# Performance work log

Hardware: AMD Instinct MI355X
Metric: run time of the kernel (lower is better)

## Reference

```python
import jax, jax.numpy as jnp
import numpy as np

N, V, T, C_IN, C_OUT, REL, H4, H5 = 256, 25, 128, 64, 64, 9, 18, 6


def setup_inputs() -> dict:
    key = jax.random.key(0)
    ks = jax.random.split(key, 12)

    def w(k, shape, fan_in):
        return (jax.random.normal(k, shape, jnp.float32) / np.sqrt(fan_in)).astype(jnp.float32)

    return {
        "x": jax.random.normal(ks[0], (N, V, T, C_IN), jnp.float32),
        "A": jax.random.uniform(ks[1], (V, V), dtype=jnp.float32),
        "W1": w(ks[2], (C_IN, REL), C_IN), "b1": jnp.zeros((REL,), jnp.float32),
        "W2": w(ks[3], (C_IN, REL), C_IN), "b2": jnp.zeros((REL,), jnp.float32),
        "W3": w(ks[4], (C_IN, REL), C_IN), "b3": jnp.zeros((REL,), jnp.float32),
        "W4a": w(ks[5], (REL, H4), REL), "b4a": jnp.zeros((H4,), jnp.float32),
        "W4b": w(ks[6], (H4, REL), H4), "b4b": jnp.zeros((REL,), jnp.float32),
        "W5a": w(ks[7], (REL, H5), REL), "b5a": jnp.zeros((H5,), jnp.float32),
        "W5b": w(ks[8], (H5, C_OUT), H5), "b5b": jnp.zeros((C_OUT,), jnp.float32),
    }


def reference(x, A, W1, b1, W2, b2, W3, b3, W4a, b4a, W4b, b4b, W5a, b5a, W5b, b5b):
    silu = jax.nn.silu
    alpha = 1.0
    # x: (N, V, T, C) channels-last; Linear projections to rel channels
    x1 = x @ W1 + b1                       # (N, V, T, R)
    x2 = x @ W2 + b2                       # (N, V, T, R)
    x3 = x @ W3 + b3                       # (N, V, T, R)
    # temporal mean (original: transpose(1,3).mean(-2))
    m1 = x1.mean(axis=2)                   # (N, V, R)
    m2 = x2.mean(axis=2)                   # (N, V, R)
    # pairwise joint affinity via broadcast difference
    rel = m1[:, :, None, :] - m2[:, None, :, :]   # (N, V, V, R)
    # small MLP (Linear4) on channel dim
    h = silu(rel @ W4a + b4a)              # (N, V, V, 18)
    h = silu(h @ W4b + b4b)                # (N, V, V, R)
    # scale + static adjacency (broadcast over batch and channels)
    h = h * alpha + A[None, :, :, None]    # (N, V, V, R)
    # einsum 'ncuv,nctv->nctu' in channels-last form: aggregate over v
    agg = jnp.einsum('nuvc,nvtc->nutc', h, x3)    # (N, V, T, R)
    # output MLP (Linear5)
    y = silu(agg @ W5a + b5a)              # (N, V, T, 6)
    y = silu(y @ W5b + b5b)                # (N, V, T, C_out)
    return y
```

## Files before the change

### kernel.cpp

```cpp
#include <hip/hip_runtime.h>
#include <hip/hip_fp16.h>

#define NN 256
#define VV 25
#define TT 128
#define CIN 64
#define CO 64
#define RR 9
#define HH4 18
#define HH5 6
#define TQ 32
#define NT 4

typedef unsigned int uint;

__device__ __forceinline__ float silu_f(float v) {
  return __fdividef(v, 1.0f + __expf(-v));
}
__device__ __forceinline__ __half2 u2h(uint u) {
  union { uint x; __half2 h; } c; c.x = u; return c.h;
}
__device__ __forceinline__ uint h2u(__half2 h) {
  union { __half2 h; uint x; } c; c.h = h; return c.x;
}

__global__ __launch_bounds__(128, 2) void k1_proj(
    const float* __restrict__ x, const float* __restrict__ W3,
    const float* __restrict__ b3, uint* __restrict__ x3g,
    float* __restrict__ xm) {
  const int blk = blockIdx.x;
  const int n = blk / VV, v = blk - n * VV;
  const int tid = threadIdx.x;
  __shared__ __align__(16) float xt[TT * 68];
  __shared__ __align__(16) float xmp[2][64];

  const float4* src = (const float4*)(x + (size_t)blk * TT * CIN);
  float4 r[16];
  #pragma unroll
  for (int k = 0; k < 16; ++k) r[k] = src[k * 128 + tid];
  #pragma unroll
  for (int k = 0; k < 16; ++k) {
    const int idx = k * 128 + tid;
    const int t = idx >> 4, c = (idx & 15) * 4;
    *(float4*)(xt + t * 68 + c) = r[k];
  }
  float4 cs = r[0];
  #pragma unroll
  for (int k = 1; k < 16; ++k) {
    cs.x += r[k].x; cs.y += r[k].y; cs.z += r[k].z; cs.w += r[k].w;
  }
  #pragma unroll
  for (int m = 16; m < 64; m <<= 1) {
    cs.x += __shfl_xor(cs.x, m); cs.y += __shfl_xor(cs.y, m);
    cs.z += __shfl_xor(cs.z, m); cs.w += __shfl_xor(cs.w, m);
  }
  if ((tid & 63) < 16) *(float4*)(&xmp[tid >> 6][(tid & 15) * 4]) = cs;
  __syncthreads();
  if (tid < 64) xm[(size_t)blk * 64 + tid] = xmp[0][tid] + xmp[1][tid];

  float acc[RR];
  #pragma unroll
  for (int j = 0; j < RR; ++j) acc[j] = b3[j];
  const float* xrow = xt + tid * 68;
  #pragma unroll
  for (int c4 = 0; c4 < 16; ++c4) {
    const float4 xv = *(const float4*)(xrow + c4 * 4);
    #pragma unroll
    for (int j = 0; j < RR; ++j) {
      acc[j] = fmaf(xv.x, W3[(c4 * 4 + 0) * RR + j], acc[j]);
      acc[j] = fmaf(xv.y, W3[(c4 * 4 + 1) * RR + j], acc[j]);
      acc[j] = fmaf(xv.z, W3[(c4 * 4 + 2) * RR + j], acc[j]);
      acc[j] = fmaf(xv.w, W3[(c4 * 4 + 3) * RR + j], acc[j]);
    }
  }
  uint w[5];
  w[0] = h2u(__floats2half2_rn(acc[0], acc[1]));
  w[1] = h2u(__floats2half2_rn(acc[2], acc[3]));
  w[2] = h2u(__floats2half2_rn(acc[4], acc[5]));
  w[3] = h2u(__floats2half2_rn(acc[6], acc[7]));
  w[4] = h2u(__floats2half2_rn(acc[8], 0.f));
  const int tq = tid >> 5, t = tid & 31;
  uint* dst = x3g + (size_t)(n * NT + tq) * (5 * VV * TQ) + v * TQ + t;
  #pragma unroll
  for (int c = 0; c < 5; ++c) dst[c * (VV * TQ)] = w[c];
}

__global__ __launch_bounds__(256, 4) void k3_out(
    const uint* __restrict__ x3g, const float* __restrict__ xm,
    const float* __restrict__ A,
    const float* __restrict__ W1, const float* __restrict__ b1,
    const float* __restrict__ W2, const float* __restrict__ b2,
    const float* __restrict__ W4a, const float* __restrict__ b4a,
    const float* __restrict__ W4b, const float* __restrict__ b4b,
    const float* __restrict__ W5a, const float* __restrict__ b5a,
    const float* __restrict__ W5b, const float* __restrict__ b5b,
    float* __restrict__ out) {
  const int bid = blockIdx.x;
  const int n = bid >> 2, tq = bid & 3;
  const int tid = threadIdx.x;
  __shared__ __align__(16) uint pool[9525];
  uint* x3s = pool;
  uint* a5s = pool + 4000;
  float* m12 = (float*)(pool + 4000);
  float* xmL = (float*)(pool + 4500);
  uint* h_lds = pool + 6400;

  {
    const uint4* xsrc = (const uint4*)(x3g + (size_t)bid * 4000);
    for (int i = tid; i < 1000; i += 256) ((uint4*)x3s)[i] = xsrc[i];
    const float4* msrc = (const float4*)(xm + (size_t)n * VV * CIN);
    for (int i = tid; i < 400; i += 256) ((float4*)xmL)[i] = msrc[i];
  }
  __syncthreads();

  for (int i = tid; i < 2 * VV * RR; i += 256) {
    const int which = (i >= VV * RR);
    const int idx = which ? i - VV * RR : i;
    const int v = idx / RR, c = idx - v * RR;
    const float* W = which ? W2 : W1;
    const float* b = which ? b2 : b1;
    const float* row = xmL + v * CIN;
    float s = 0.f;
    #pragma unroll
    for (int k = 0; k < CIN; ++k) s = fmaf(row[k], W[k * RR + c], s);
    m12[(which * VV + v) * 10 + c] = s * (1.0f / TT) + b[c];
  }
  __syncthreads();

  for (int p = tid; p < VV * VV; p += 256) {
    const int u = p / VV, v2 = p - u * VV;
    float rel[RR];
    #pragma unroll
    for (int j = 0; j < RR; ++j) rel[j] = m12[u * 10 + j] - m12[(VV + v2) * 10 + j];
    float t1[HH4];
    #pragma unroll
    for (int k = 0; k < HH4; ++k) {
      float s = b4a[k];
      #pragma unroll
      for (int j = 0; j < RR; ++j) s = fmaf(rel[j], W4a[j * HH4 + k], s);
      t1[k] = silu_f(s);
    }
    const float av = A[u * VV + v2];
    float hc[RR];
    #pragma unroll
    for (int j = 0; j < RR; ++j) {
      float s = b4b[j];
      #pragma unroll
      for (int k = 0; k < HH4; ++k) s = fmaf(t1[k], W4b[k * RR + j], s);
      hc[j] = silu_f(s) + av;
    }
    uint* hp = h_lds + p * 5;
    hp[0] = h2u(__floats2half2_rn(hc[0], hc[1]));
    hp[1] = h2u(__floats2half2_rn(hc[2], hc[3]));
    hp[2] = h2u(__floats2half2_rn(hc[4], hc[5]));
    hp[3] = h2u(__floats2half2_rn(hc[6], hc[7]));
    hp[4] = h2u(__floats2half2_rn(hc[8], 0.f));
  }
  __syncthreads();

  for (int p = tid; p < VV * TQ; p += 256) {
    const int u = p >> 5, t = p & 31;
    const uint* hr = h_lds + u * VV * 5;
    __half2 c0 = u2h(0u), c1 = c0, c2 = c0, c3 = c0, c4 = c0;
    #pragma unroll 5
    for (int v2 = 0; v2 < VV; ++v2) {
      const int xo = v2 * TQ + t;
      const uint x0 = x3s[xo];
      const uint x1 = x3s[xo + 800];
      const uint x2 = x3s[xo + 1600];
      const uint x3 = x3s[xo + 2400];
      const uint x4 = x3s[xo + 3200];
      const uint* hv = hr + v2 * 5;
      c0 = __hfma2(u2h(hv[0]), u2h(x0), c0);
      c1 = __hfma2(u2h(hv[1]), u2h(x1), c1);
      c2 = __hfma2(u2h(hv[2]), u2h(x2), c2);
      c3 = __hfma2(u2h(hv[3]), u2h(x3), c3);
      c4 = __hfma2(u2h(hv[4]), u2h(x4), c4);
    }
    float ag[RR];
    ag[0] = __low2float(c0); ag[1] = __high2float(c0);
    ag[2] = __low2float(c1); ag[3] = __high2float(c1);
    ag[4] = __low2float(c2); ag[5] = __high2float(c2);
    ag[6] = __low2float(c3); ag[7] = __high2float(c3);
    ag[8] = __low2float(c4);
    float a5v[HH5];
    #pragma unroll
    for (int k = 0; k < HH5; ++k) {
      float s = b5a[k];
      #pragma unroll
      for (int j = 0; j < RR; ++j) s = fmaf(ag[j], W5a[j * HH5 + k], s);
      a5v[k] = silu_f(s);
    }
    a5s[p * 3 + 0] = h2u(__floats2half2_rn(a5v[0], a5v[1]));
    a5s[p * 3 + 1] = h2u(__floats2half2_rn(a5v[2], a5v[3]));
    a5s[p * 3 + 2] = h2u(__floats2half2_rn(a5v[4], a5v[5]));
  }
  __syncthreads();

  const int cq = (tid & 15) * 4;
  float4 wb[HH5];
  #pragma unroll
  for (int k = 0; k < HH5; ++k) wb[k] = *(const float4*)(W5b + k * CO + cq);
  const float4 bb = *(const float4*)(b5b + cq);
  for (int it = 0; it < (VV * TQ) / 16; ++it) {
    const int q = it * 16 + (tid >> 4);
    const int u = q >> 5, t = q & 31;
    const __half2 p01 = u2h(a5s[q * 3 + 0]);
    const __half2 p23 = u2h(a5s[q * 3 + 1]);
    const __half2 p45 = u2h(a5s[q * 3 + 2]);
    const float a0 = __low2float(p01), a1 = __high2float(p01);
    const float a2 = __low2float(p23), a3 = __high2float(p23);
    const float a4 = __low2float(p45), a5 = __high2float(p45);
    float4 y;
    y.x = silu_f(bb.x + a0 * wb[0].x + a1 * wb[1].x + a2 * wb[2].x +
                 a3 * wb[3].x + a4 * wb[4].x + a5 * wb[5].x);
    y.y = silu_f(bb.y + a0 * wb[0].y + a1 * wb[1].y + a2 * wb[2].y +
                 a3 * wb[3].y + a4 * wb[4].y + a5 * wb[5].y);
    y.z = silu_f(bb.z + a0 * wb[0].z + a1 * wb[1].z + a2 * wb[2].z +
                 a3 * wb[3].z + a4 * wb[4].z + a5 * wb[5].z);
    y.w = silu_f(bb.w + a0 * wb[0].w + a1 * wb[1].w + a2 * wb[2].w +
                 a3 * wb[3].w + a4 * wb[4].w + a5 * wb[5].w);
    float* orow = out +
        ((size_t)(n * VV + u) * TT + tq * TQ + t) * CO + cq;
    *(float4*)orow = y;
  }
}

extern "C" void kernel_launch(void* const* d_in, const int* in_sizes, int n_in,
                              void* d_out, int out_size, void* d_ws, size_t ws_size,
                              hipStream_t stream) {
  const float* x   = (const float*)d_in[0];
  const float* A   = (const float*)d_in[1];
  const float* W1  = (const float*)d_in[2];
  const float* b1  = (const float*)d_in[3];
  const float* W2  = (const float*)d_in[4];
  const float* b2  = (const float*)d_in[5];
  const float* W3  = (const float*)d_in[6];
  const float* b3  = (const float*)d_in[7];
  const float* W4a = (const float*)d_in[8];
  const float* b4a = (const float*)d_in[9];
  const float* W4b = (const float*)d_in[10];
  const float* b4b = (const float*)d_in[11];
  const float* W5a = (const float*)d_in[12];
  const float* b5a = (const float*)d_in[13];
  const float* W5b = (const float*)d_in[14];
  const float* b5b = (const float*)d_in[15];
  float* out = (float*)d_out;

  char* ws = (char*)d_ws;
  uint*  x3g = (uint*)ws;
  float* xm  = (float*)(ws + 16384000);

  hipLaunchKernelGGL(k1_proj, dim3(NN * VV), dim3(128), 0, stream,
                     x, W3, b3, x3g, xm);
  hipLaunchKernelGGL(k3_out, dim3(NN * NT), dim3(256), 0, stream,
                     x3g, xm, A, W1, b1, W2, b2, W4a, b4a, W4b, b4b,
                     W5a, b5a, W5b, b5b, out);
}
```

Measured before the change: 174.4 us.

## Split fused output kernel into separate h, aggregation, and output-MLP kernels

The single k3_out kernel is split into three launches. k2_h computes the per-batch pairwise affinity h once per batch instead of once per time quarter and stores it to global memory. k3_agg does the aggregation and first output layer and writes a 6-wide intermediate to global memory. k4_out runs the final 6-to-64 layer with a higher occupancy bound. This removes the fourfold redundant h computation and lowers LDS pressure, at the cost of extra launches and an intermediate written to and read back from global memory.

```diff
diff --git a/kernel.cpp b/kernel.cpp
--- a/kernel.cpp
+++ b/kernel.cpp
@@ -85,53 +85,37 @@
   for (int c = 0; c < 5; ++c) dst[c * (VV * TQ)] = w[c];
 }
 
-__global__ __launch_bounds__(256, 4) void k3_out(
-    const uint* __restrict__ x3g, const float* __restrict__ xm,
-    const float* __restrict__ A,
+__global__ __launch_bounds__(128) void k2_h(
+    const float* __restrict__ xm, const float* __restrict__ A,
     const float* __restrict__ W1, const float* __restrict__ b1,
     const float* __restrict__ W2, const float* __restrict__ b2,
     const float* __restrict__ W4a, const float* __restrict__ b4a,
     const float* __restrict__ W4b, const float* __restrict__ b4b,
-    const float* __restrict__ W5a, const float* __restrict__ b5a,
-    const float* __restrict__ W5b, const float* __restrict__ b5b,
-    float* __restrict__ out) {
-  const int bid = blockIdx.x;
-  const int n = bid >> 2, tq = bid & 3;
-  const int tid = threadIdx.x;
-  __shared__ __align__(16) uint pool[9525];
-  uint* x3s = pool;
-  uint* a5s = pool + 4000;
-  float* m12 = (float*)(pool + 4000);
-  float* xmL = (float*)(pool + 4500);
-  uint* h_lds = pool + 6400;
-
-  {
-    const uint4* xsrc = (const uint4*)(x3g + (size_t)bid * 4000);
-    for (int i = tid; i < 1000; i += 256) ((uint4*)x3s)[i] = xsrc[i];
-    const float4* msrc = (const float4*)(xm + (size_t)n * VV * CIN);
-    for (int i = tid; i < 400; i += 256) ((float4*)xmL)[i] = msrc[i];
-  }
-  __syncthreads();
-
-  for (int i = tid; i < 2 * VV * RR; i += 256) {
+    uint* __restrict__ h2g) {
+  const int n = blockIdx.x;
+  const int tid = threadIdx.x;
+  __shared__ float m1[VV][RR + 1];
+  __shared__ float m2[VV][RR + 1];
+  const float* xmn = xm + (size_t)n * VV * CIN;
+  for (int i = tid; i < 2 * VV * RR; i += 128) {
     const int which = (i >= VV * RR);
     const int idx = which ? i - VV * RR : i;
     const int v = idx / RR, c = idx - v * RR;
     const float* W = which ? W2 : W1;
     const float* b = which ? b2 : b1;
-    const float* row = xmL + v * CIN;
+    const float* row = xmn + v * CIN;
     float s = 0.f;
     #pragma unroll
     for (int k = 0; k < CIN; ++k) s = fmaf(row[k], W[k * RR + c], s);
-    m12[(which * VV + v) * 10 + c] = s * (1.0f / TT) + b[c];
+    s = s * (1.0f / TT) + b[c];
+    if (which) m2[v][c] = s; else m1[v][c] = s;
   }
   __syncthreads();
-
-  for (int p = tid; p < VV * VV; p += 256) {
+  for (int p = tid; p < VV * VV; p += 128) {
     const int u = p / VV, v2 = p - u * VV;
     float rel[RR];
     #pragma unroll
-    for (int j = 0; j < RR; ++j) rel[j] = m12[u * 10 + j] - m12[(VV + v2) * 10 + j];
+    for (int j = 0; j < RR; ++j) rel[j] = m1[u][j] - m2[v2][j];
     float t1[HH4];
     #pragma unroll
     for (int k = 0; k < HH4; ++k) {
@@ -149,18 +133,36 @@
       for (int k = 0; k < HH4; ++k) s = fmaf(t1[k], W4b[k * RR + j], s);
       hc[j] = silu_f(s) + av;
     }
-    uint* hp = h_lds + p * 5;
+    uint* hp = h2g + (size_t)n * (VV * VV * 5) + (size_t)p * 5;
     hp[0] = h2u(__floats2half2_rn(hc[0], hc[1]));
     hp[1] = h2u(__floats2half2_rn(hc[2], hc[3]));
     hp[2] = h2u(__floats2half2_rn(hc[4], hc[5]));
     hp[3] = h2u(__floats2half2_rn(hc[6], hc[7]));
     hp[4] = h2u(__floats2half2_rn(hc[8], 0.f));
   }
+}
+
+__global__ __launch_bounds__(256, 4) void k3_agg(
+    const uint* __restrict__ x3g, const uint* __restrict__ h2g,
+    const float* __restrict__ W5a, const float* __restrict__ b5a,
+    float* __restrict__ a5g) {
+  const int bid = blockIdx.x;
+  const int n = bid >> 2, tq = bid & 3;
+  const int tid = threadIdx.x;
+  __shared__ __align__(16) uint x3s[5 * VV * TQ];
+  __shared__ __align__(16) uint h2s[VV * VV * 5];
+
+  {
+    const uint4* xsrc = (const uint4*)(x3g + (size_t)bid * 4000);
+    for (int i = tid; i < 1000; i += 256) ((uint4*)x3s)[i] = xsrc[i];
+    const uint* hsrc = h2g + (size_t)n * (VV * VV * 5);
+    for (int i = tid; i < VV * VV * 5; i += 256) h2s[i] = hsrc[i];
+  }
   __syncthreads();
 
   for (int p = tid; p < VV * TQ; p += 256) {
     const int u = p >> 5, t = p & 31;
-    const uint* hr = h_lds + u * VV * 5;
+    const uint* hr = h2s + u * (VV * 5);
     __half2 c0 = u2h(0u), c1 = c0, c2 = c0, c3 = c0, c4 = c0;
     #pragma unroll 5
     for (int v2 = 0; v2 < VV; ++v2) {
@@ -191,38 +193,39 @@
       for (int j = 0; j < RR; ++j) s = fmaf(ag[j], W5a[j * HH5 + k], s);
       a5v[k] = silu_f(s);
     }
-    a5s[p * 3 + 0] = h2u(__floats2half2_rn(a5v[0], a5v[1]));
-    a5s[p * 3 + 1] = h2u(__floats2half2_rn(a5v[2], a5v[3]));
-    a5s[p * 3 + 2] = h2u(__floats2half2_rn(a5v[4], a5v[5]));
-  }
-  __syncthreads();
-
+    const size_t row = ((size_t)(n * VV + u)) * TT + tq * TQ + t;
+    float* dst = a5g + row * 8;
+    *(float4*)dst = make_float4(a5v[0], a5v[1], a5v[2], a5v[3]);
+    *(float2*)(dst + 4) = make_float2(a5v[4], a5v[5]);
+  }
+}
+
+__global__ __launch_bounds__(256, 8) void k4_out(
+    const float* __restrict__ a5g,
+    const float* __restrict__ W5b, const float* __restrict__ b5b,
+    float* __restrict__ out) {
+  const int tid = threadIdx.x;
   const int cq = (tid & 15) * 4;
   float4 wb[HH5];
   #pragma unroll
   for (int k = 0; k < HH5; ++k) wb[k] = *(const float4*)(W5b + k * CO + cq);
   const float4 bb = *(const float4*)(b5b + cq);
-  for (int it = 0; it < (VV * TQ) / 16; ++it) {
-    const int q = it * 16 + (tid >> 4);
-    const int u = q >> 5, t = q & 31;
-    const __half2 p01 = u2h(a5s[q * 3 + 0]);
-    const __half2 p23 = u2h(a5s[q * 3 + 1]);
-    const __half2 p45 = u2h(a5s[q * 3 + 2]);
-    const float a0 = __low2float(p01), a1 = __high2float(p01);
-    const float a2 = __low2float(p23), a3 = __high2float(p23);
-    const float a4 = __low2float(p45), a5 = __high2float(p45);
+  const size_t row0 = (size_t)blockIdx.x * 400 + (tid >> 4);
+  #pragma unroll 2
+  for (int it = 0; it < 25; ++it) {
+    const size_t r = row0 + (size_t)it * 16;
+    const float4 aA = *(const float4*)(a5g + r * 8);
+    const float2 aB = *(const float2*)(a5g + r * 8 + 4);
     float4 y;
-    y.x = silu_f(bb.x + a0 * wb[0].x + a1 * wb[1].x + a2 * wb[2].x +
-                 a3 * wb[3].x + a4 * wb[4].x + a5 * wb[5].x);
-    y.y = silu_f(bb.y + a0 * wb[0].y + a1 * wb[1].y + a2 * wb[2].y +
-                 a3 * wb[3].y + a4 * wb[4].y + a5 * wb[5].y);
-    y.z = silu_f(bb.z + a0 * wb[0].z + a1 * wb[1].z + a2 * wb[2].z +
-                 a3 * wb[3].z + a4 * wb[4].z + a5 * wb[5].z);
-    y.w = silu_f(bb.w + a0 * wb[0].w + a1 * wb[1].w + a2 * wb[2].w +
-                 a3 * wb[3].w + a4 * wb[4].w + a5 * wb[5].w);
-    float* orow = out +
-        ((size_t)(n * VV + u) * TT + tq * TQ + t) * CO + cq;
-    *(float4*)orow = y;
+    y.x = silu_f(bb.x + aA.x * wb[0].x + aA.y * wb[1].x + aA.z * wb[2].x +
+                 aA.w * wb[3].x + aB.x * wb[4].x + aB.y * wb[5].x);
+    y.y = silu_f(bb.y + aA.x * wb[0].y + aA.y * wb[1].y + aA.z * wb[2].y +
+                 aA.w * wb[3].y + aB.x * wb[4].y + aB.y * wb[5].y);
+    y.z = silu_f(bb.z + aA.x * wb[0].z + aA.y * wb[1].z + aA.z * wb[2].z +
+                 aA.w * wb[3].z + aB.x * wb[4].z + aB.y * wb[5].z);
+    y.w = silu_f(bb.w + aA.x * wb[0].w + aA.y * wb[1].w + aA.z * wb[2].w +
+                 aA.w * wb[3].w + aB.x * wb[4].w + aB.y * wb[5].w);
+    *(float4*)(out + r * CO + cq) = y;
   }
 }
 
@@ -250,10 +253,15 @@
   char* ws = (char*)d_ws;
   uint*  x3g = (uint*)ws;
   float* xm  = (float*)(ws + 16384000);
+  uint*  h2g = (uint*)(ws + 16384000 + 1638400);
+  float* a5g = (float*)(ws + 16384000 + 1638400 + 3200000);
 
   hipLaunchKernelGGL(k1_proj, dim3(NN * VV), dim3(128), 0, stream,
                      x, W3, b3, x3g, xm);
-  hipLaunchKernelGGL(k3_out, dim3(NN * NT), dim3(256), 0, stream,
-                     x3g, xm, A, W1, b1, W2, b2, W4a, b4a, W4b, b4b,
-                     W5a, b5a, W5b, b5b, out);
-}
+  hipLaunchKernelGGL(k2_h, dim3(NN), dim3(128), 0, stream,
+                     xm, A, W1, b1, W2, b2, W4a, b4a, W4b, b4b, h2g);
+  hipLaunchKernelGGL(k3_agg, dim3(NN * NT), dim3(256), 0, stream,
+                     x3g, h2g, W5a, b5a, a5g);
+  hipLaunchKernelGGL(k4_out, dim3(2048), dim3(256), 0, stream,
+                     a5g, W5b, b5b, out);
+}
```

Result: no change. 174.1 us (-0.2%).

## Split pairwise affinity MLP into its own kernel and halve output time tiles

Applied to the files above, without the earlier changes.

Moves the per-batch m1/m2 projection and pairwise MLP out of the output kernel into a new per-batch kernel that writes the half-precision affinity matrix to workspace. Before, every time-quarter block recomputed it redundantly. The output kernel now uses 16-step time tiles over 8 blocks per batch, reading the affinity directly from global memory, which gives more, lighter blocks. The projection kernel stages x in LDS as half precision to shrink shared memory, at some accuracy cost. The change also adds an extra kernel launch and a global round trip for the affinity data.

```diff
diff --git a/kernel.cpp b/kernel.cpp
--- a/kernel.cpp
+++ b/kernel.cpp
@@ -9,8 +9,8 @@
 #define RR 9
 #define HH4 18
 #define HH5 6
-#define TQ 32
-#define NT 4
+#define TQ 16
+#define NT 8
 
 typedef unsigned int uint;
 
@@ -24,14 +24,14 @@
   union { __half2 h; uint x; } c; c.h = h; return c.x;
 }
 
-__global__ __launch_bounds__(128, 2) void k1_proj(
+__global__ __launch_bounds__(128) void k1_proj(
     const float* __restrict__ x, const float* __restrict__ W3,
     const float* __restrict__ b3, uint* __restrict__ x3g,
     float* __restrict__ xm) {
   const int blk = blockIdx.x;
   const int n = blk / VV, v = blk - n * VV;
   const int tid = threadIdx.x;
-  __shared__ __align__(16) float xt[TT * 68];
+  __shared__ __align__(16) __half xt[TT * 66];
   __shared__ __align__(16) float xmp[2][64];
 
   const float4* src = (const float4*)(x + (size_t)blk * TT * CIN);
@@ -42,7 +42,8 @@
   for (int k = 0; k < 16; ++k) {
     const int idx = k * 128 + tid;
     const int t = idx >> 4, c = (idx & 15) * 4;
-    *(float4*)(xt + t * 68 + c) = r[k];
+    *(__half2*)(&xt[t * 66 + c])     = __floats2half2_rn(r[k].x, r[k].y);
+    *(__half2*)(&xt[t * 66 + c + 2]) = __floats2half2_rn(r[k].z, r[k].w);
   }
   float4 cs = r[0];
   #pragma unroll
@@ -61,16 +62,15 @@
   float acc[RR];
   #pragma unroll
   for (int j = 0; j < RR; ++j) acc[j] = b3[j];
-  const float* xrow = xt + tid * 68;
-  #pragma unroll
-  for (int c4 = 0; c4 < 16; ++c4) {
-    const float4 xv = *(const float4*)(xrow + c4 * 4);
+  const __half* xrow = xt + tid * 66;
+  #pragma unroll 8
+  for (int c2 = 0; c2 < 32; ++c2) {
+    const __half2 hv = *(const __half2*)(&xrow[c2 * 2]);
+    const float x0 = __low2float(hv), x1 = __high2float(hv);
     #pragma unroll
     for (int j = 0; j < RR; ++j) {
-      acc[j] = fmaf(xv.x, W3[(c4 * 4 + 0) * RR + j], acc[j]);
-      acc[j] = fmaf(xv.y, W3[(c4 * 4 + 1) * RR + j], acc[j]);
-      acc[j] = fmaf(xv.z, W3[(c4 * 4 + 2) * RR + j], acc[j]);
-      acc[j] = fmaf(xv.w, W3[(c4 * 4 + 3) * RR + j], acc[j]);
+      acc[j] = fmaf(x0, W3[(c2 * 2 + 0) * RR + j], acc[j]);
+      acc[j] = fmaf(x1, W3[(c2 * 2 + 1) * RR + j], acc[j]);
     }
   }
   uint w[5];
@@ -79,59 +79,43 @@
   w[2] = h2u(__floats2half2_rn(acc[4], acc[5]));
   w[3] = h2u(__floats2half2_rn(acc[6], acc[7]));
   w[4] = h2u(__floats2half2_rn(acc[8], 0.f));
-  const int tq = tid >> 5, t = tid & 31;
+  const int tq = tid >> 4, t = tid & 15;
   uint* dst = x3g + (size_t)(n * NT + tq) * (5 * VV * TQ) + v * TQ + t;
   #pragma unroll
   for (int c = 0; c < 5; ++c) dst[c * (VV * TQ)] = w[c];
 }
 
-__global__ __launch_bounds__(256, 4) void k3_out(
-    const uint* __restrict__ x3g, const float* __restrict__ xm,
-    const float* __restrict__ A,
+__global__ __launch_bounds__(128) void k2_h(
+    const float* __restrict__ xm, const float* __restrict__ A,
     const float* __restrict__ W1, const float* __restrict__ b1,
     const float* __restrict__ W2, const float* __restrict__ b2,
     const float* __restrict__ W4a, const float* __restrict__ b4a,
     const float* __restrict__ W4b, const float* __restrict__ b4b,
-    const float* __restrict__ W5a, const float* __restrict__ b5a,
-    const float* __restrict__ W5b, const float* __restrict__ b5b,
-    float* __restrict__ out) {
-  const int bid = blockIdx.x;
-  const int n = bid >> 2, tq = bid & 3;
+    uint* __restrict__ h2g) {
+  const int n = blockIdx.x;
   const int tid = threadIdx.x;
-  __shared__ __align__(16) uint pool[9525];
-  uint* x3s = pool;
-  uint* a5s = pool + 4000;
-  float* m12 = (float*)(pool + 4000);
-  float* xmL = (float*)(pool + 4500);
-  uint* h_lds = pool + 6400;
-
-  {
-    const uint4* xsrc = (const uint4*)(x3g + (size_t)bid * 4000);
-    for (int i = tid; i < 1000; i += 256) ((uint4*)x3s)[i] = xsrc[i];
-    const float4* msrc = (const float4*)(xm + (size_t)n * VV * CIN);
-    for (int i = tid; i < 400; i += 256) ((float4*)xmL)[i] = msrc[i];
-  }
-  __syncthreads();
-
-  for (int i = tid; i < 2 * VV * RR; i += 256) {
+  __shared__ float m1[VV][RR + 1];
+  __shared__ float m2[VV][RR + 1];
+  const float* xmn = xm + (size_t)n * VV * CIN;
+  for (int i = tid; i < 2 * VV * RR; i += 128) {
     const int which = (i >= VV * RR);
     const int idx = which ? i - VV * RR : i;
     const int v = idx / RR, c = idx - v * RR;
     const float* W = which ? W2 : W1;
     const float* b = which ? b2 : b1;
-    const float* row = xmL + v * CIN;
+    const float* row = xmn + v * CIN;
     float s = 0.f;
     #pragma unroll
     for (int k = 0; k < CIN; ++k) s = fmaf(row[k], W[k * RR + c], s);
-    m12[(which * VV + v) * 10 + c] = s * (1.0f / TT) + b[c];
-  }
-  __syncthreads();
-
-  for (int p = tid; p < VV * VV; p += 256) {
+    s = s * (1.0f / TT) + b[c];
+    if (which) m2[v][c] = s; else m1[v][c] = s;
+  }
+  __syncthreads();
+  for (int p = tid; p < VV * VV; p += 128) {
     const int u = p / VV, v2 = p - u * VV;
     float rel[RR];
     #pragma unroll
-    for (int j = 0; j < RR; ++j) rel[j] = m12[u * 10 + j] - m12[(VV + v2) * 10 + j];
+    for (int j = 0; j < RR; ++j) rel[j] = m1[u][j] - m2[v2][j];
     float t1[HH4];
     #pragma unroll
     for (int k = 0; k < HH4; ++k) {
@@ -149,27 +133,46 @@
       for (int k = 0; k < HH4; ++k) s = fmaf(t1[k], W4b[k * RR + j], s);
       hc[j] = silu_f(s) + av;
     }
-    uint* hp = h_lds + p * 5;
+    uint* hp = h2g + (size_t)n * (VV * VV * 5) + (size_t)p * 5;
     hp[0] = h2u(__floats2half2_rn(hc[0], hc[1]));
     hp[1] = h2u(__floats2half2_rn(hc[2], hc[3]));
     hp[2] = h2u(__floats2half2_rn(hc[4], hc[5]));
     hp[3] = h2u(__floats2half2_rn(hc[6], hc[7]));
     hp[4] = h2u(__floats2half2_rn(hc[8], 0.f));
   }
+}
+
+__global__ __launch_bounds__(256) void k3_out(
+    const uint* __restrict__ x3g, const uint* __restrict__ h2g,
+    const float* __restrict__ W5a, const float* __restrict__ b5a,
+    const float* __restrict__ W5b, const float* __restrict__ b5b,
+    float* __restrict__ out) {
+  const int bid = blockIdx.x;
+  const int n = bid >> 3, tq = bid & 7;
+  const int tid = threadIdx.x;
+  __shared__ __align__(16) uint x3s[5 * VV * TQ];
+  __shared__ __align__(16) uint a5s[VV * TQ * 3];
+
+  {
+    const uint4* xsrc = (const uint4*)(x3g + (size_t)bid * (5 * VV * TQ));
+    for (int i = tid; i < (5 * VV * TQ) / 4; i += 256)
+      ((uint4*)x3s)[i] = xsrc[i];
+  }
   __syncthreads();
 
   for (int p = tid; p < VV * TQ; p += 256) {
-    const int u = p >> 5, t = p & 31;
-    const uint* hr = h_lds + u * VV * 5;
+    const int u = p >> 4, t = p & 15;
+    const uint* hr = h2g + (size_t)n * (VV * VV * 5) + u * (VV * 5);
+    const uint* xr = x3s + t;
     __half2 c0 = u2h(0u), c1 = c0, c2 = c0, c3 = c0, c4 = c0;
     #pragma unroll 5
     for (int v2 = 0; v2 < VV; ++v2) {
-      const int xo = v2 * TQ + t;
-      const uint x0 = x3s[xo];
-      const uint x1 = x3s[xo + 800];
-      const uint x2 = x3s[xo + 1600];
-      const uint x3 = x3s[xo + 2400];
-      const uint x4 = x3s[xo + 3200];
+      const int xo = v2 * TQ;
+      const uint x0 = xr[xo];
+      const uint x1 = xr[xo + 400];
+      const uint x2 = xr[xo + 800];
+      const uint x3 = xr[xo + 1200];
+      const uint x4 = xr[xo + 1600];
       const uint* hv = hr + v2 * 5;
       c0 = __hfma2(u2h(hv[0]), u2h(x0), c0);
       c1 = __hfma2(u2h(hv[1]), u2h(x1), c1);
@@ -204,7 +207,7 @@
   const float4 bb = *(const float4*)(b5b + cq);
   for (int it = 0; it < (VV * TQ) / 16; ++it) {
     const int q = it * 16 + (tid >> 4);
-    const int u = q >> 5, t = q & 31;
+    const int u = q >> 4, t = q & 15;
     const __half2 p01 = u2h(a5s[q * 3 + 0]);
     const __half2 p23 = u2h(a5s[q * 3 + 1]);
     const __half2 p45 = u2h(a5s[q * 3 + 2]);
@@ -250,10 +253,12 @@
   char* ws = (char*)d_ws;
   uint*  x3g = (uint*)ws;
   float* xm  = (float*)(ws + 16384000);
+  uint*  h2g = (uint*)(ws + 16384000 + 1638400);
 
   hipLaunchKernelGGL(k1_proj, dim3(NN * VV), dim3(128), 0, stream,
                      x, W3, b3, x3g, xm);
+  hipLaunchKernelGGL(k2_h, dim3(NN), dim3(128), 0, stream,
+                     xm, A, W1, b1, W2, b2, W4a, b4a, W4b, b4b, h2g);
   hipLaunchKernelGGL(k3_out, dim3(NN * NT), dim3(256), 0, stream,
-                     x3g, xm, A, W1, b1, W2, b2, W4a, b4a, W4b, b4b,
-                     W5a, b5a, W5b, b5b, out);
-}
+                     x3g, h2g, W5a, b5a, W5b, b5b, out);
+}
```

New measurement: 152.4 us. 1.14x faster.
